# Kernel tuning notes

Hardware: AMD Instinct MI355X
Metric: run time of the kernel (lower is better)

The kernel has to match this reference:

```python
import jax, jax.numpy as jnp
import numpy as np

B, S, D, H = 8, 2048, 512, 8
NEG = -1e9


def setup_inputs() -> dict:
    key = jax.random.key(0)
    ks = jax.random.split(key, 12)
    inp = {
        "v": jax.random.normal(ks[0], (B, S, D), jnp.float32),
        "k": jax.random.normal(ks[1], (B, S, D), jnp.float32),
        "q": jax.random.normal(ks[2], (B, S, D), jnp.float32),
    }
    # pad_mask: 1.0 where key position is padding ([B,1,1,S]); random valid lengths
    lens = jax.random.randint(ks[3], (B,), S // 2, S + 1)
    inp["pad_mask"] = (jnp.arange(S)[None, :] >= lens[:, None]).astype(jnp.float32)[:, None, None, :]
    # head_mask: causal look-ahead mask, 1.0 above diagonal ([1,1,S,S])
    inp["head_mask"] = jnp.triu(jnp.ones((S, S), jnp.float32), k=1)[None, None]
    # Dense layer params (Keras Dense: y = x @ W + b)
    sc = 1.0 / np.sqrt(D)
    inp["Wq"] = jax.random.normal(ks[4], (D, D), jnp.float32) * sc
    inp["bq"] = jnp.zeros((D,), jnp.float32)
    inp["Wk"] = jax.random.normal(ks[5], (D, D), jnp.float32) * sc
    inp["bk"] = jnp.zeros((D,), jnp.float32)
    inp["Wv"] = jax.random.normal(ks[6], (D, D), jnp.float32) * sc
    inp["bv"] = jnp.zeros((D,), jnp.float32)
    inp["Wo"] = jax.random.normal(ks[7], (D, D), jnp.float32) * sc
    inp["bo"] = jnp.zeros((D,), jnp.float32)
    inp["num_heads"] = H
    return inp


def reference(v, k, q, pad_mask, head_mask, Wq, bq, Wk, bk, Wv, bv, Wo, bo, num_heads):
    b, s, d = q.shape
    depth = d // num_heads

    def split_heads(x):  # [b,s,d] -> [b,h,s,depth]
        return x.reshape(b, -1, num_heads, depth).transpose(0, 2, 1, 3)

    qh = split_heads(q @ Wq + bq)
    kh = split_heads(k @ Wk + bk)
    vh = split_heads(v @ Wv + bv)

    scale = 1.0 / jnp.sqrt(jnp.asarray(depth, qh.dtype))
    scores = jnp.einsum("bhqd,bhkd->bhqk", qh, kh) * scale
    scores = scores + pad_mask * NEG + head_mask * NEG
    attn = jax.nn.softmax(scores, axis=-1)
    ctx = jnp.einsum("bhqk,bhkd->bhqd", attn, vh)
    concat = ctx.transpose(0, 2, 1, 3).reshape(b, -1, d)
    return concat @ Wo + bo
```

## Files before the change

### kernel.cpp

```cpp
#include <hip/hip_runtime.h>

#define B_ 8
#define S_ 2048
#define D_ 512
#define H_ 8
#define HD_ 64

typedef __attribute__((ext_vector_type(8))) short short8;
typedef __attribute__((ext_vector_type(4))) short short4v;
typedef __attribute__((ext_vector_type(4))) float f32x4;
typedef __attribute__((ext_vector_type(16))) float f32x16;
typedef __attribute__((ext_vector_type(8))) __bf16 bf16x8;
typedef __attribute__((ext_vector_type(4))) unsigned uint4v;

__device__ __forceinline__ short f2bf(float f) {
    union { float f; unsigned u; } x; x.f = f;
    unsigned r = x.u + 0x7fffu + ((x.u >> 16) & 1u);
    return (short)(r >> 16);
}

__device__ __forceinline__ unsigned cvtpk(float a, float b) {
    unsigned r;
    asm("v_cvt_pk_bf16_f32 %0, %1, %2" : "=v"(r) : "v"(a), "v"(b));
    return r;
}

__device__ __forceinline__ void gl16(const void* g, void* l) {
    __builtin_amdgcn_global_load_lds(
        (const __attribute__((address_space(1))) unsigned*)g,
        (__attribute__((address_space(3))) unsigned*)l, 16, 0, 0);
}

__device__ __forceinline__ f32x4 mfma16(short8 a, short8 b, f32x4 c) {
    return __builtin_amdgcn_mfma_f32_16x16x32_bf16(
        __builtin_bit_cast(bf16x8, a), __builtin_bit_cast(bf16x8, b), c, 0, 0, 0);
}

__device__ __forceinline__ f32x16 mfma32(short8 a, short8 b, f32x16 c) {
    return __builtin_amdgcn_mfma_f32_32x32x16_bf16(
        __builtin_bit_cast(bf16x8, a), __builtin_bit_cast(bf16x8, b), c, 0, 0, 0);
}

__device__ __forceinline__ f32x16 zero16() {
    f32x16 z;
    #pragma unroll
    for (int i = 0; i < 16; ++i) z[i] = 0.f;
    return z;
}

__global__ __launch_bounds__(256) void prep_wt(
    const float* __restrict__ W0, const float* __restrict__ W1,
    const float* __restrict__ W2, const float* __restrict__ W3,
    short* __restrict__ T0, short* __restrict__ T1,
    short* __restrict__ T2, short* __restrict__ T3)
{
    const float* W = (blockIdx.z == 0) ? W0 : (blockIdx.z == 1) ? W1 : (blockIdx.z == 2) ? W2 : W3;
    short* T = (blockIdx.z == 0) ? T0 : (blockIdx.z == 1) ? T1 : (blockIdx.z == 2) ? T2 : T3;
    __shared__ float t_s[64][65];
    const int tid = threadIdx.x;
    const int k0 = blockIdx.x * 64, n0 = blockIdx.y * 64;
    const int col = tid & 63, rg = tid >> 6;
    #pragma unroll
    for (int j = 0; j < 16; ++j) {
        const int row = rg * 16 + j;
        t_s[row][col] = W[(size_t)(k0 + row) * D_ + n0 + col];
    }
    __syncthreads();
    #pragma unroll
    for (int j = 0; j < 16; ++j) {
        const int nn = rg * 16 + j;
        const int kswz = ((((col >> 3) ^ (nn & 7)) << 3) | (col & 7));
        T[(size_t)(n0 + nn) * D_ + k0 + kswz] = f2bf(t_s[col][nn]);
    }
}

__global__ __launch_bounds__(512) void qkv_gemm(
    const float* __restrict__ q_in, const float* __restrict__ k_in, const float* __restrict__ v_in,
    const short* __restrict__ wtq, const short* __restrict__ wtk, const short* __restrict__ wtv,
    const float* __restrict__ bq, const float* __restrict__ bk, const float* __restrict__ bv,
    short* __restrict__ qh, short* __restrict__ kh, short* __restrict__ vtb, float qscale)
{
    const int id = blockIdx.x;
    const int xcd = id & 7;
    const int slot = id >> 3;
    const int n0 = (slot & 3) * 128;
    const int pidx = xcd * 48 + (slot >> 2);
    const int z = pidx >> 7;
    const int m0 = (pidx & 127) * 128;

    const float* Ain = (z == 0) ? q_in : (z == 1) ? k_in : v_in;
    const short* Wt  = (z == 0) ? wtq  : (z == 1) ? wtk  : wtv;
    const float* bias = (z == 0) ? bq : (z == 1) ? bk : bv;
    short* Cout = (z == 0) ? qh : (z == 1) ? kh : vtb;
    const float osc = (z == 0) ? qscale : 1.0f;
    const int N = D_, K = D_;

    __shared__ __align__(16) short a_s[128 * 72];
    __shared__ __align__(16) short b_s[2][128 * 64];

    const int tid = threadIdx.x;
    const int lane = tid & 63, wave = tid >> 6;
    const int wr = wave >> 2, wc = wave & 3;
    const int lr = lane & 15, lg = lane >> 4;
    const int srow = tid >> 3, sch = (tid & 7) * 8;
    const int lsw = lr & 7;

    f32x4 acc[4][2] = {};

    f32x4 fa[4];
    {
        const f32x4* ap0 = (const f32x4*)(Ain + (size_t)(m0 + srow) * K + sch);
        fa[0] = ap0[0]; fa[1] = ap0[1];
        const f32x4* ap1 = (const f32x4*)(Ain + (size_t)(m0 + srow + 64) * K + sch);
        fa[2] = ap1[0]; fa[3] = ap1[1];
        const short* bsrc = Wt + (size_t)(n0 + wave * 8 + (lane >> 3)) * K + (lane & 7) * 8;
        gl16(bsrc, &b_s[0][wave * 512]);
        gl16(bsrc + (size_t)64 * K, &b_s[0][4096 + wave * 512]);
    }

    int cur = 0;
    for (int k0 = 0; k0 < K; k0 += 64) {
        __syncthreads();
        {
            const uint4v u0 = { cvtpk(fa[0][0], fa[0][1]), cvtpk(fa[0][2], fa[0][3]),
                                cvtpk(fa[1][0], fa[1][1]), cvtpk(fa[1][2], fa[1][3]) };
            *(short8*)&a_s[srow * 72 + sch] = __builtin_bit_cast(short8, u0);
            const uint4v u1 = { cvtpk(fa[2][0], fa[2][1]), cvtpk(fa[2][2], fa[2][3]),
                                cvtpk(fa[3][0], fa[3][1]), cvtpk(fa[3][2], fa[3][3]) };
            *(short8*)&a_s[(srow + 64) * 72 + sch] = __builtin_bit_cast(short8, u1);
        }
        __syncthreads();
        if (k0 + 64 < K) {
            const f32x4* ap0 = (const f32x4*)(Ain + (size_t)(m0 + srow) * K + k0 + 64 + sch);
            fa[0] = ap0[0]; fa[1] = ap0[1];
            const f32x4* ap1 = (const f32x4*)(Ain + (size_t)(m0 + srow + 64) * K + k0 + 64 + sch);
            fa[2] = ap1[0]; fa[3] = ap1[1];
            const short* bsrc = Wt + (size_t)(n0 + wave * 8 + (lane >> 3)) * K + k0 + 64 + (lane & 7) * 8;
            gl16(bsrc, &b_s[cur ^ 1][wave * 512]);
            gl16(bsrc + (size_t)64 * K, &b_s[cur ^ 1][4096 + wave * 512]);
        }

        #pragma unroll
        for (int kc = 0; kc < 2; ++kc) {
            short8 af[4], bf[2];
            #pragma unroll
            for (int m = 0; m < 4; ++m)
                af[m] = *(const short8*)&a_s[(wr * 64 + m * 16 + lr) * 72 + kc * 32 + lg * 8];
            #pragma unroll
            for (int n = 0; n < 2; ++n)
                bf[n] = *(const short8*)&b_s[cur][(wc * 32 + n * 16 + lr) * 64 + (((kc * 4 + lg) ^ lsw) << 3)];
            __builtin_amdgcn_s_setprio(1);
            #pragma unroll
            for (int m = 0; m < 4; ++m)
                #pragma unroll
                for (int n = 0; n < 2; ++n)
                    acc[m][n] = mfma16(af[m], bf[n], acc[m][n]);
            __builtin_amdgcn_s_setprio(0);
        }
        cur ^= 1;
    }

    float bvv[2];
    #pragma unroll
    for (int n = 0; n < 2; ++n) bvv[n] = bias[n0 + wc * 32 + n * 16 + lr];

    if (z == 2) {
        #pragma unroll
        for (int m = 0; m < 4; ++m) {
            const int row0 = m0 + wr * 64 + m * 16 + lg * 4;
            const int bb = row0 >> 11, s0 = row0 & (S_ - 1);
            #pragma unroll
            for (int n = 0; n < 2; ++n) {
                const int col = n0 + wc * 32 + n * 16 + lr;
                uint2 wv;
                wv.x = cvtpk(acc[m][n][0] + bvv[n], acc[m][n][1] + bvv[n]);
                wv.y = cvtpk(acc[m][n][2] + bvv[n], acc[m][n][3] + bvv[n]);
                *(uint2*)(Cout + ((size_t)col * B_ + bb) * S_ + s0) = wv;
            }
        }
    } else {
        #pragma unroll
        for (int m = 0; m < 4; ++m)
            #pragma unroll
            for (int i = 0; i < 4; ++i) {
                const size_t row = m0 + wr * 64 + m * 16 + lg * 4 + i;
                #pragma unroll
                for (int n = 0; n < 2; ++n) {
                    const int col = n0 + wc * 32 + n * 16 + lr;
                    Cout[row * N + col] = f2bf((acc[m][n][i] + bvv[n]) * osc);
                }
            }
    }
}

__global__ __launch_bounds__(512) void out_gemm(
    const short* __restrict__ Ain, const short* __restrict__ Wt,
    const float* __restrict__ bias, float* __restrict__ Cout)
{
    const int id = blockIdx.x;
    const int xcd = id & 7;
    const int slot = id >> 3;
    const int n0 = (slot & 3) * 128;
    const int m0 = (xcd * 16 + (slot >> 2)) * 128;
    const int N = D_, K = D_;

    __shared__ __align__(16) short a_s[2][128 * 64];
    __shared__ __align__(16) short b_s[2][128 * 64];

    const int tid = threadIdx.x;
    const int lane = tid & 63, wave = tid >> 6;
    const int wr = wave >> 2, wc = wave & 3;
    const int lr = lane & 15, lg = lane >> 4;
    const int lsw = lr & 7;

    f32x4 acc[4][2] = {};

    {
        const short* asrc = Ain + (size_t)(m0 + wave * 8 + (lane >> 3)) * K + (lane & 7) * 8;
        gl16(asrc, &a_s[0][wave * 512]);
        gl16(asrc + (size_t)64 * K, &a_s[0][4096 + wave * 512]);
        const short* bsrc = Wt + (size_t)(n0 + wave * 8 + (lane >> 3)) * K + (lane & 7) * 8;
        gl16(bsrc, &b_s[0][wave * 512]);
        gl16(bsrc + (size_t)64 * K, &b_s[0][4096 + wave * 512]);
    }

    int cur = 0;
    for (int k0 = 0; k0 < K; k0 += 64) {
        __syncthreads();
        if (k0 + 64 < K) {
            const short* asrc = Ain + (size_t)(m0 + wave * 8 + (lane >> 3)) * K + k0 + 64 + (lane & 7) * 8;
            gl16(asrc, &a_s[cur ^ 1][wave * 512]);
            gl16(asrc + (size_t)64 * K, &a_s[cur ^ 1][4096 + wave * 512]);
            const short* bsrc = Wt + (size_t)(n0 + wave * 8 + (lane >> 3)) * K + k0 + 64 + (lane & 7) * 8;
            gl16(bsrc, &b_s[cur ^ 1][wave * 512]);
            gl16(bsrc + (size_t)64 * K, &b_s[cur ^ 1][4096 + wave * 512]);
        }

        #pragma unroll
        for (int kc = 0; kc < 2; ++kc) {
            short8 af[4], bf[2];
            #pragma unroll
            for (int m = 0; m < 4; ++m)
                af[m] = *(const short8*)&a_s[cur][(wr * 64 + m * 16 + lr) * 64 + (((kc * 4 + lg) ^ lsw) << 3)];
            #pragma unroll
            for (int n = 0; n < 2; ++n)
                bf[n] = *(const short8*)&b_s[cur][(wc * 32 + n * 16 + lr) * 64 + (((kc * 4 + lg) ^ lsw) << 3)];
            __builtin_amdgcn_s_setprio(1);
            #pragma unroll
            for (int m = 0; m < 4; ++m)
                #pragma unroll
                for (int n = 0; n < 2; ++n)
                    acc[m][n] = mfma16(af[m], bf[n], acc[m][n]);
            __builtin_amdgcn_s_setprio(0);
        }
        cur ^= 1;
    }

    float bvv[2];
    #pragma unroll
    for (int n = 0; n < 2; ++n) bvv[n] = bias[n0 + wc * 32 + n * 16 + lr];
    #pragma unroll
    for (int m = 0; m < 4; ++m)
        #pragma unroll
        for (int i = 0; i < 4; ++i) {
            const size_t row = m0 + wr * 64 + m * 16 + lg * 4 + i;
            #pragma unroll
            for (int n = 0; n < 2; ++n)
                Cout[row * N + n0 + wc * 32 + n * 16 + lr] = acc[m][n][i] + bvv[n];
        }
}

__global__ __launch_bounds__(128, 3) void attn_k(
    const short* __restrict__ qh, const short* __restrict__ kh,
    const short* __restrict__ vt, const float* __restrict__ pad_mask,
    short* __restrict__ ctx)
{
    const int tid = threadIdx.x;
    const int lane = tid & 63, w = tid >> 6;
    const int l31 = lane & 31, hi = lane >> 5;
    const int id = blockIdx.x;
    const int h = id & 7;
    const int b = (id >> 3) & 7;
    const int pair = id >> 6;
    const int NT = S_ / 64;

    __shared__ __align__(16) short k_s[64 * 72];
    __shared__ __align__(16) short vt_s[64 * 68];
    __shared__ float red_s[2];

    const float* pb = pad_mask + (size_t)b * S_;
    {
        const f32x4* pv4 = (const f32x4*)pb;
        float psum = 0.f;
        #pragma unroll
        for (int j = 0; j < 4; ++j) {
            const f32x4 a = pv4[tid * 4 + j];
            psum += a[0] + a[1] + a[2] + a[3];
        }
        for (int off = 1; off < 64; off <<= 1) psum += __shfl_xor(psum, off);
        if (lane == 0) red_s[w] = psum;
    }
    __syncthreads();
    const int len = S_ - (int)(red_s[0] + red_s[1] + 0.5f);

    const int srow = tid >> 1, sc0 = (tid & 1) * 32;
    const short* kbase = kh + ((size_t)b * S_ + srow) * D_ + h * HD_ + sc0;
    const short* vbase = vt + ((size_t)(h * HD_ + srow) * B_ + b) * S_ + sc0;

    for (int half = 0; half < 2; ++half) {
        const int qt = half ? (NT - 1 - pair) : pair;
        const int q0 = qt * 64;
        const int kt_end = min(qt, (len - 1) >> 6);

        const int qrow = q0 + 2 * l31 + w;
        const short* qptr = qh + ((size_t)b * S_ + qrow) * D_ + h * HD_ + hi * 8;
        short8 qf[4];
        #pragma unroll
        for (int dd = 0; dd < 4; ++dd) qf[dd] = *(const short8*)(qptr + dd * 16);

        f32x16 accA = zero16(), accB = zero16();
        float m_r = -1e30f, l_r = 0.f;
        const int kmax = min(qrow, len - 1);

        short8 kv[4], vv[4];
        #pragma unroll
        for (int p = 0; p < 4; ++p) {
            kv[p] = ((const short8*)kbase)[p];
            vv[p] = ((const short8*)vbase)[p];
        }

        for (int kt = 0; kt <= kt_end; ++kt) {
            __syncthreads();
            #pragma unroll
            for (int p = 0; p < 4; ++p)
                *(short8*)&k_s[srow * 72 + sc0 + p * 8] = kv[p];
            #pragma unroll
            for (int p = 0; p < 4; ++p) {
                *(short4v*)&vt_s[srow * 68 + sc0 + p * 8]     = __builtin_shufflevector(vv[p], vv[p], 0, 1, 2, 3);
                *(short4v*)&vt_s[srow * 68 + sc0 + p * 8 + 4] = __builtin_shufflevector(vv[p], vv[p], 4, 5, 6, 7);
            }
            __syncthreads();
            if (kt < kt_end) {
                const short* kp = kbase + (size_t)(kt + 1) * 64 * D_;
                const short* vp = vbase + (kt + 1) * 64;
                #pragma unroll
                for (int p = 0; p < 4; ++p) {
                    kv[p] = ((const short8*)kp)[p];
                    vv[p] = ((const short8*)vp)[p];
                }
            }

            f32x16 scA = zero16(), scB = zero16();
            __builtin_amdgcn_s_setprio(1);
            #pragma unroll
            for (int dd = 0; dd < 4; ++dd) {
                const short8 kfA = *(const short8*)&k_s[l31 * 72 + dd * 16 + hi * 8];
                const short8 kfB = *(const short8*)&k_s[(32 + l31) * 72 + dd * 16 + hi * 8];
                scA = mfma32(kfA, qf[dd], scA);
                scB = mfma32(kfB, qf[dd], scB);
            }
            __builtin_amdgcn_s_setprio(0);

            const bool needmask = (kt == qt) || (kt * 64 + 63 >= len);
            if (needmask) {
                #pragma unroll
                for (int reg = 0; reg < 16; ++reg) {
                    const int koff = kt * 64 + (reg & 3) + 8 * (reg >> 2) + 4 * hi;
                    if (koff > kmax)      scA[reg] = -1e30f;
                    if (koff + 32 > kmax) scB[reg] = -1e30f;
                }
            }

            float m8[8], m4[4];
            #pragma unroll
            for (int i = 0; i < 8; ++i) m8[i] = fmaxf(fmaxf(scA[i], scA[i + 8]), fmaxf(scB[i], scB[i + 8]));
            #pragma unroll
            for (int i = 0; i < 4; ++i) m4[i] = fmaxf(m8[i], m8[i + 4]);
            float mt = fmaxf(fmaxf(m4[0], m4[1]), fmaxf(m4[2], m4[3]));
            mt = fmaxf(mt, __shfl_xor(mt, 32));
            const bool nogrow = __all(mt <= m_r);
            const float mn = nogrow ? m_r : fmaxf(m_r, mt);

            #pragma unroll
            for (int i = 0; i < 16; ++i) {
                scA[i] = __builtin_amdgcn_exp2f(scA[i] - mn);
                scB[i] = __builtin_amdgcn_exp2f(scB[i] - mn);
            }
            float s8[8], s4[4];
            #pragma unroll
            for (int i = 0; i < 8; ++i) s8[i] = (scA[i] + scA[i + 8]) + (scB[i] + scB[i + 8]);
            #pragma unroll
            for (int i = 0; i < 4; ++i) s4[i] = s8[i] + s8[i + 4];
            float rs = (s4[0] + s4[1]) + (s4[2] + s4[3]);
            rs += __shfl_xor(rs, 32);

            if (nogrow) {
                l_r += rs;
            } else {
                const float fac = __builtin_amdgcn_exp2f(m_r - mn);
                l_r = l_r * fac + rs;
                m_r = mn;
                #pragma unroll
                for (int reg = 0; reg < 16; ++reg) { accA[reg] *= fac; accB[reg] *= fac; }
            }

            unsigned pw[4][4];
            #pragma unroll
            for (int kk = 0; kk < 4; ++kk) {
                const int g = kk & 1;
                unsigned w0, w1, w2, w3;
                if (kk < 2) {
                    w0 = cvtpk(scA[8 * g + 0], scA[8 * g + 1]);
                    w1 = cvtpk(scA[8 * g + 2], scA[8 * g + 3]);
                    w2 = cvtpk(scA[8 * g + 4], scA[8 * g + 5]);
                    w3 = cvtpk(scA[8 * g + 6], scA[8 * g + 7]);
                } else {
                    w0 = cvtpk(scB[8 * g + 0], scB[8 * g + 1]);
                    w1 = cvtpk(scB[8 * g + 2], scB[8 * g + 3]);
                    w2 = cvtpk(scB[8 * g + 4], scB[8 * g + 5]);
                    w3 = cvtpk(scB[8 * g + 6], scB[8 * g + 7]);
                }
                asm("v_permlane32_swap_b32 %0, %1" : "+v"(w0), "+v"(w2));
                asm("v_permlane32_swap_b32 %0, %1" : "+v"(w1), "+v"(w3));
                pw[kk][0] = w0; pw[kk][1] = w1; pw[kk][2] = w2; pw[kk][3] = w3;
            }

            __builtin_amdgcn_s_setprio(1);
            #pragma unroll
            for (int kk = 0; kk < 4; ++kk) {
                const uint4v u = { pw[kk][0], pw[kk][1], pw[kk][2], pw[kk][3] };
                const short8 pf = __builtin_bit_cast(short8, u);
                const short4v a0 = *(const short4v*)&vt_s[l31 * 68 + kk * 16 + 8 * hi];
                const short4v a1 = *(const short4v*)&vt_s[l31 * 68 + kk * 16 + 8 * hi + 4];
                const short8 afA = __builtin_shufflevector(a0, a1, 0, 1, 2, 3, 4, 5, 6, 7);
                accA = mfma32(afA, pf, accA);
                const short4v b0 = *(const short4v*)&vt_s[(32 + l31) * 68 + kk * 16 + 8 * hi];
                const short4v b1 = *(const short4v*)&vt_s[(32 + l31) * 68 + kk * 16 + 8 * hi + 4];
                const short8 afB = __builtin_shufflevector(b0, b1, 0, 1, 2, 3, 4, 5, 6, 7);
                accB = mfma32(afB, pf, accB);
            }
            __builtin_amdgcn_s_setprio(0);
        }

        const float li = __builtin_amdgcn_rcpf(l_r);
        const int rsw = qrow & 7;
        short* cpb = ctx + ((size_t)b * S_ + qrow) * D_ + h * HD_ + 4 * hi;
        #pragma unroll
        for (int g = 0; g < 4; ++g) {
            uint2 wa;
            wa.x = cvtpk(accA[4 * g + 0] * li, accA[4 * g + 1] * li);
            wa.y = cvtpk(accA[4 * g + 2] * li, accA[4 * g + 3] * li);
            *(uint2*)(cpb + ((g ^ rsw) << 3)) = wa;
            uint2 wb;
            wb.x = cvtpk(accB[4 * g + 0] * li, accB[4 * g + 1] * li);
            wb.y = cvtpk(accB[4 * g + 2] * li, accB[4 * g + 3] * li);
            *(uint2*)(cpb + (((g + 4) ^ rsw) << 3)) = wb;
        }
    }
}

extern "C" void kernel_launch(void* const* d_in, const int* in_sizes, int n_in,
                              void* d_out, int out_size, void* d_ws, size_t ws_size,
                              hipStream_t stream)
{
    const float* v_in = (const float*)d_in[0];
    const float* k_in = (const float*)d_in[1];
    const float* q_in = (const float*)d_in[2];
    const float* pad  = (const float*)d_in[3];
    const float* Wq = (const float*)d_in[5];  const float* bq = (const float*)d_in[6];
    const float* Wk = (const float*)d_in[7];  const float* bk = (const float*)d_in[8];
    const float* Wv = (const float*)d_in[9];  const float* bv = (const float*)d_in[10];
    const float* Wo = (const float*)d_in[11]; const float* bo = (const float*)d_in[12];

    const size_t elems = (size_t)B_ * S_ * D_;
    const size_t welems = (size_t)D_ * D_;
    short* qh  = (short*)d_ws;
    short* kh  = qh + elems;
    short* vtb = kh + elems;
    short* ctx = vtb + elems;
    short* wtq = ctx + elems;
    short* wtk = wtq + welems;
    short* wtv = wtk + welems;
    short* wto = wtv + welems;

    prep_wt<<<dim3(D_ / 64, D_ / 64, 4), dim3(256), 0, stream>>>(Wq, Wk, Wv, Wo, wtq, wtk, wtv, wto);

    const float qscale = 0.125f * 1.4426950408889634f;
    qkv_gemm<<<dim3(1536), dim3(512), 0, stream>>>(
        q_in, k_in, v_in, wtq, wtk, wtv, bq, bk, bv, qh, kh, vtb, qscale);

    attn_k<<<dim3(1024), dim3(128), 0, stream>>>(qh, kh, vtb, pad, ctx);

    out_gemm<<<dim3(512), dim3(512), 0, stream>>>(ctx, wto, bo, (float*)d_out);
}
```

Baseline: 130.4 us.

## Split KV range across two waves with per-wave LDS tiles and merge softmax

The attention kernel now gives each block 32 query rows instead of 64 and splits the key tiles between the two waves (even and odd tiles). Each wave has its own LDS K/V buffer, so the per-tile block barriers go away. At the end the two partial softmax states are merged through LDS. The grid doubles to 2048 blocks and the launch bounds drop to 2 blocks per CU, which allows more registers for the larger prefetch buffers. The cost is extra merge work, reloading each K/V tile for twice as many query tiles, and lower occupancy.

```diff
diff --git a/kernel.cpp b/kernel.cpp
--- a/kernel.cpp
+++ b/kernel.cpp
@@ -270,7 +270,7 @@
         }
 }
 
-__global__ __launch_bounds__(128, 3) void attn_k(
+__global__ __launch_bounds__(128, 2) void attn_k(
     const short* __restrict__ qh, const short* __restrict__ kh,
     const short* __restrict__ vt, const float* __restrict__ pad_mask,
     short* __restrict__ ctx)
@@ -281,38 +281,40 @@
     const int id = blockIdx.x;
     const int h = id & 7;
     const int b = (id >> 3) & 7;
-    const int pair = id >> 6;
-    const int NT = S_ / 64;
-
-    __shared__ __align__(16) short k_s[64 * 72];
-    __shared__ __align__(16) short vt_s[64 * 68];
-    __shared__ float red_s[2];
-
-    const float* pb = pad_mask + (size_t)b * S_;
+    const int p = id >> 6;
+
+    __shared__ __align__(16) short k_s[2][64 * 72];
+    __shared__ __align__(16) short vt_s[2][64 * 68];
+
+    float psum = 0.f;
     {
-        const f32x4* pv4 = (const f32x4*)pb;
-        float psum = 0.f;
-        #pragma unroll
-        for (int j = 0; j < 4; ++j) {
-            const f32x4 a = pv4[tid * 4 + j];
-            psum += a[0] + a[1] + a[2] + a[3];
-        }
+        const f32x4* pv4 = (const f32x4*)(pad_mask + (size_t)b * S_);
+        #pragma unroll
+        for (int j = 0; j < 8; ++j) {
+            const f32x4 a = pv4[lane * 8 + j];
+            psum += (a[0] + a[1]) + (a[2] + a[3]);
+        }
+        #pragma unroll
         for (int off = 1; off < 64; off <<= 1) psum += __shfl_xor(psum, off);
-        if (lane == 0) red_s[w] = psum;
-    }
-    __syncthreads();
-    const int len = S_ - (int)(red_s[0] + red_s[1] + 0.5f);
-
-    const int srow = tid >> 1, sc0 = (tid & 1) * 32;
-    const short* kbase = kh + ((size_t)b * S_ + srow) * D_ + h * HD_ + sc0;
-    const short* vbase = vt + ((size_t)(h * HD_ + srow) * B_ + b) * S_ + sc0;
+    }
+    const int len = S_ - (int)(psum + 0.5f);
+    const int lenT = (len - 1) >> 6;
+
+    const short* kbase = kh + ((size_t)b * S_ + lane) * D_ + h * HD_;
+    const short* vbase = vt + ((size_t)(h * HD_ + lane) * B_ + b) * S_;
+
+    float* accx = (float*)&k_s[0][0];
+    float* mx = (float*)&vt_s[0][0];
+    float* lx = mx + 128;
 
     for (int half = 0; half < 2; ++half) {
-        const int qt = half ? (NT - 1 - pair) : pair;
-        const int q0 = qt * 64;
-        const int kt_end = min(qt, (len - 1) >> 6);
-
-        const int qrow = q0 + 2 * l31 + w;
+        const int qt = half ? (63 - p) : p;
+        const int q0 = qt * 32;
+        const int dt = qt >> 1;
+        const int kt_end = min(dt, lenT);
+        const int qrow = q0 + l31;
+        const int kmax = min(qrow, len - 1);
+
         const short* qptr = qh + ((size_t)b * S_ + qrow) * D_ + h * HD_ + hi * 8;
         short8 qf[4];
         #pragma unroll
@@ -320,33 +322,33 @@
 
         f32x16 accA = zero16(), accB = zero16();
         float m_r = -1e30f, l_r = 0.f;
-        const int kmax = min(qrow, len - 1);
-
-        short8 kv[4], vv[4];
-        #pragma unroll
-        for (int p = 0; p < 4; ++p) {
-            kv[p] = ((const short8*)kbase)[p];
-            vv[p] = ((const short8*)vbase)[p];
-        }
-
-        for (int kt = 0; kt <= kt_end; ++kt) {
-            __syncthreads();
-            #pragma unroll
-            for (int p = 0; p < 4; ++p)
-                *(short8*)&k_s[srow * 72 + sc0 + p * 8] = kv[p];
-            #pragma unroll
-            for (int p = 0; p < 4; ++p) {
-                *(short4v*)&vt_s[srow * 68 + sc0 + p * 8]     = __builtin_shufflevector(vv[p], vv[p], 0, 1, 2, 3);
-                *(short4v*)&vt_s[srow * 68 + sc0 + p * 8 + 4] = __builtin_shufflevector(vv[p], vv[p], 4, 5, 6, 7);
-            }
-            __syncthreads();
-            if (kt < kt_end) {
-                const short* kp = kbase + (size_t)(kt + 1) * 64 * D_;
-                const short* vp = vbase + (kt + 1) * 64;
+
+        int kt = w;
+        short8 kv[8], vv[8];
+        if (kt <= kt_end) {
+            const short* kp = kbase + (size_t)kt * 64 * D_;
+            const short* vp = vbase + kt * 64;
+            #pragma unroll
+            for (int pp = 0; pp < 8; ++pp) {
+                kv[pp] = *(const short8*)(kp + pp * 8);
+                vv[pp] = *(const short8*)(vp + pp * 8);
+            }
+        }
+
+        for (; kt <= kt_end; kt += 2) {
+            #pragma unroll
+            for (int pp = 0; pp < 8; ++pp)
+                *(short8*)&k_s[w][lane * 72 + pp * 8] = kv[pp];
+            #pragma unroll
+            for (int pp = 0; pp < 8; ++pp)
+                *(short8*)&vt_s[w][lane * 68 + pp * 8] = vv[pp];
+            if (kt + 2 <= kt_end) {
+                const short* kp = kbase + (size_t)(kt + 2) * 64 * D_;
+                const short* vp = vbase + (kt + 2) * 64;
                 #pragma unroll
-                for (int p = 0; p < 4; ++p) {
-                    kv[p] = ((const short8*)kp)[p];
-                    vv[p] = ((const short8*)vp)[p];
+                for (int pp = 0; pp < 8; ++pp) {
+                    kv[pp] = *(const short8*)(kp + pp * 8);
+                    vv[pp] = *(const short8*)(vp + pp * 8);
                 }
             }
 
@@ -354,15 +356,14 @@
             __builtin_amdgcn_s_setprio(1);
             #pragma unroll
             for (int dd = 0; dd < 4; ++dd) {
-                const short8 kfA = *(const short8*)&k_s[l31 * 72 + dd * 16 + hi * 8];
-                const short8 kfB = *(const short8*)&k_s[(32 + l31) * 72 + dd * 16 + hi * 8];
+                const short8 kfA = *(const short8*)&k_s[w][l31 * 72 + dd * 16 + hi * 8];
+                const short8 kfB = *(const short8*)&k_s[w][(32 + l31) * 72 + dd * 16 + hi * 8];
                 scA = mfma32(kfA, qf[dd], scA);
                 scB = mfma32(kfB, qf[dd], scB);
             }
             __builtin_amdgcn_s_setprio(0);
 
-            const bool needmask = (kt == qt) || (kt * 64 + 63 >= len);
-            if (needmask) {
+            if (kt == dt || kt * 64 + 63 >= len) {
                 #pragma unroll
                 for (int reg = 0; reg < 16; ++reg) {
                     const int koff = kt * 64 + (reg & 3) + 8 * (reg >> 2) + 4 * hi;
@@ -430,32 +431,55 @@
             for (int kk = 0; kk < 4; ++kk) {
                 const uint4v u = { pw[kk][0], pw[kk][1], pw[kk][2], pw[kk][3] };
                 const short8 pf = __builtin_bit_cast(short8, u);
-                const short4v a0 = *(const short4v*)&vt_s[l31 * 68 + kk * 16 + 8 * hi];
-                const short4v a1 = *(const short4v*)&vt_s[l31 * 68 + kk * 16 + 8 * hi + 4];
+                const short4v a0 = *(const short4v*)&vt_s[w][l31 * 68 + kk * 16 + 8 * hi];
+                const short4v a1 = *(const short4v*)&vt_s[w][l31 * 68 + kk * 16 + 8 * hi + 4];
                 const short8 afA = __builtin_shufflevector(a0, a1, 0, 1, 2, 3, 4, 5, 6, 7);
                 accA = mfma32(afA, pf, accA);
-                const short4v b0 = *(const short4v*)&vt_s[(32 + l31) * 68 + kk * 16 + 8 * hi];
-                const short4v b1 = *(const short4v*)&vt_s[(32 + l31) * 68 + kk * 16 + 8 * hi + 4];
+                const short4v b0 = *(const short4v*)&vt_s[w][(32 + l31) * 68 + kk * 16 + 8 * hi];
+                const short4v b1 = *(const short4v*)&vt_s[w][(32 + l31) * 68 + kk * 16 + 8 * hi + 4];
                 const short8 afB = __builtin_shufflevector(b0, b1, 0, 1, 2, 3, 4, 5, 6, 7);
                 accB = mfma32(afB, pf, accB);
             }
             __builtin_amdgcn_s_setprio(0);
         }
 
-        const float li = __builtin_amdgcn_rcpf(l_r);
-        const int rsw = qrow & 7;
-        short* cpb = ctx + ((size_t)b * S_ + qrow) * D_ + h * HD_ + 4 * hi;
-        #pragma unroll
-        for (int g = 0; g < 4; ++g) {
-            uint2 wa;
-            wa.x = cvtpk(accA[4 * g + 0] * li, accA[4 * g + 1] * li);
-            wa.y = cvtpk(accA[4 * g + 2] * li, accA[4 * g + 3] * li);
-            *(uint2*)(cpb + ((g ^ rsw) << 3)) = wa;
-            uint2 wb;
-            wb.x = cvtpk(accB[4 * g + 0] * li, accB[4 * g + 1] * li);
-            wb.y = cvtpk(accB[4 * g + 2] * li, accB[4 * g + 3] * li);
-            *(uint2*)(cpb + (((g + 4) ^ rsw) << 3)) = wb;
-        }
+        __syncthreads();
+        mx[w * 64 + lane] = m_r;
+        lx[w * 64 + lane] = l_r;
+        __syncthreads();
+        const float mo = mx[(w ^ 1) * 64 + lane];
+        const float lo = lx[(w ^ 1) * 64 + lane];
+        const float mj = fmaxf(m_r, mo);
+        const float facS = __builtin_amdgcn_exp2f(m_r - mj);
+        const float facO = __builtin_amdgcn_exp2f(mo - mj);
+        if (w == 1) {
+            #pragma unroll
+            for (int i = 0; i < 16; ++i) accx[i * 64 + lane] = accA[i] * facS;
+            #pragma unroll
+            for (int i = 0; i < 16; ++i) accx[(16 + i) * 64 + lane] = accB[i] * facS;
+        }
+        __syncthreads();
+        if (w == 0) {
+            const float li = __builtin_amdgcn_rcpf(l_r * facS + lo * facO);
+            const int rsw = qrow & 7;
+            short* cpb = ctx + ((size_t)b * S_ + qrow) * D_ + h * HD_ + 4 * hi;
+            #pragma unroll
+            for (int g = 0; g < 4; ++g) {
+                float o0 = (accA[4 * g + 0] * facS + accx[(4 * g + 0) * 64 + lane]) * li;
+                float o1 = (accA[4 * g + 1] * facS + accx[(4 * g + 1) * 64 + lane]) * li;
+                float o2 = (accA[4 * g + 2] * facS + accx[(4 * g + 2) * 64 + lane]) * li;
+                float o3 = (accA[4 * g + 3] * facS + accx[(4 * g + 3) * 64 + lane]) * li;
+                uint2 wa; wa.x = cvtpk(o0, o1); wa.y = cvtpk(o2, o3);
+                *(uint2*)(cpb + ((g ^ rsw) << 3)) = wa;
+                float p0 = (accB[4 * g + 0] * facS + accx[(16 + 4 * g + 0) * 64 + lane]) * li;
+                float p1 = (accB[4 * g + 1] * facS + accx[(16 + 4 * g + 1) * 64 + lane]) * li;
+                float p2 = (accB[4 * g + 2] * facS + accx[(16 + 4 * g + 2) * 64 + lane]) * li;
+                float p3 = (accB[4 * g + 3] * facS + accx[(16 + 4 * g + 3) * 64 + lane]) * li;
+                uint2 wb; wb.x = cvtpk(p0, p1); wb.y = cvtpk(p2, p3);
+                *(uint2*)(cpb + (((g + 4) ^ rsw) << 3)) = wb;
+            }
+        }
+        __syncthreads();
     }
 }
 
@@ -489,7 +513,7 @@
     qkv_gemm<<<dim3(1536), dim3(512), 0, stream>>>(
         q_in, k_in, v_in, wtq, wtk, wtv, bq, bk, bv, qh, kh, vtb, qscale);
 
-    attn_k<<<dim3(1024), dim3(128), 0, stream>>>(qh, kh, vtb, pad, ctx);
+    attn_k<<<dim3(2048), dim3(128), 0, stream>>>(qh, kh, vtb, pad, ctx);
 
     out_gemm<<<dim3(512), dim3(512), 0, stream>>>(ctx, wto, bo, (float*)d_out);
 }
```

Result: slower. 206.0 us (+58.0%).
